# Kernel tuning notes

Measured on AMD Instinct MI355X. Metric: run time of the kernel, lower is better.

Reference implementation:

```python
import jax, jax.numpy as jnp
import numpy as np

B, N = 16, 64
EMB, CDIM, NL = 32, 24, 3      # emb_dim, cloud_dim, number of degrees l=0..2 (cloudord)
NBASIS, H, RADIUS = 10, 150, 2.0
BETA = 5.0                     # rescaled_act.Softplus(beta=5)


def sp(x):
    return jax.nn.softplus(BETA * x) / BETA


def cosine_basis(r):
    # CosineBasisModel: cos^2 bumps on centers linspace(0, max_radius, nbasis)
    centers = jnp.linspace(0.0, RADIUS, NBASIS).astype(r.dtype)
    step = RADIUS / (NBASIS - 1)
    d = (r[..., None] - centers) / step
    return jnp.where(jnp.abs(d) < 1.0, jnp.cos(0.5 * jnp.pi * d) ** 2, 0.0)


def sph_harm(u):
    # real spherical harmonics l=0,1,2 on unit vectors u[...,3]
    x, y, z = u[..., 0], u[..., 1], u[..., 2]
    Y0 = jnp.full(u.shape[:-1] + (1,), 0.28209479177387814, u.dtype)
    c1 = 0.4886025119029199
    Y1 = c1 * jnp.stack([y, z, x], -1)
    c2a, c2b, c2c = 1.0925484305920792, 0.31539156525252005, 0.5462742152960396
    Y2 = jnp.stack([c2a * x * y, c2a * y * z, c2b * (3 * z * z - 1.0),
                    c2a * x * z, c2c * (x * x - y * y)], -1)
    return [Y0, Y1, Y2]


def setup_inputs() -> dict:
    key = jax.random.key(0)
    ks = jax.random.split(key, 16)
    d = {}
    d['xyz'] = jax.random.normal(ks[0], (B, N, 3), jnp.float32)
    d['Z'] = jax.random.randint(ks[1], (B, N), 0, 6)
    d['body23'] = jax.random.normal(ks[2], (B, N, 3), jnp.float32)
    # embedding table (6 species)
    d['emb_W'] = jax.random.normal(ks[3], (6, EMB), jnp.float32) * 0.1
    # radial model MLP: NBASIS -> 150 -> 150 -> 150 -> NL*CDIM*EMB
    ROUT = NL * CDIM * EMB
    d['rW0'] = jax.random.normal(ks[4], (NBASIS, H), jnp.float32) / np.sqrt(NBASIS)
    d['rb0'] = jnp.zeros((H,), jnp.float32)
    d['rW1'] = jax.random.normal(ks[5], (H, H), jnp.float32) / np.sqrt(H)
    d['rb1'] = jnp.zeros((H,), jnp.float32)
    d['rW2'] = jax.random.normal(ks[6], (H, H), jnp.float32) / np.sqrt(H)
    d['rb2'] = jnp.zeros((H,), jnp.float32)
    d['rW3'] = jax.random.normal(ks[7], (H, ROUT), jnp.float32) / np.sqrt(H)
    d['rb3'] = jnp.zeros((ROUT,), jnp.float32)
    # AtomResiduals (1 block) on 219 channels
    CR = CDIM * NL * NL + 3  # 219
    d['res_W'] = jax.random.normal(ks[8], (CR, CR), jnp.float32) / np.sqrt(CR)
    d['res_b'] = jnp.zeros((CR,), jnp.float32)
    # collate: Linear(438,128) + BatchNorm1d(128)
    d['c_W'] = jax.random.normal(ks[9], (2 * CR, 128), jnp.float32) / np.sqrt(2 * CR)
    d['c_b'] = jnp.zeros((128,), jnp.float32)
    d['bn_g'] = jnp.ones((128,), jnp.float32)
    d['bn_b'] = jnp.zeros((128,), jnp.float32)
    # output layer
    d['o_W'] = jax.random.normal(ks[10], (128, 1), jnp.float32) / np.sqrt(128.0)
    d['o_b'] = jnp.zeros((1,), jnp.float32)
    return d


def reference(xyz, Z, body23, emb_W, rW0, rb0, rW1, rb1, rW2, rb2, rW3, rb3,
              res_W, res_b, c_W, c_b, bn_g, bn_b, o_W, o_b):
    f = emb_W[Z]                                        # [B,N,EMB] atom embeddings
    diff = xyz[:, :, None, :] - xyz[:, None, :, :]      # [B,N,N,3]
    r = jnp.sqrt(jnp.sum(diff * diff, -1) + 1e-12)      # [B,N,N]
    mask = ((r < RADIUS) & (r > 1e-6)).astype(f.dtype)  # neighbors within radius, no self
    u = diff / r[..., None]
    Ys = sph_harm(u)                                    # [ [B,N,N,1], [..,3], [..,5] ]
    # radial model on all pairs
    h = sp(cosine_basis(r) @ rW0 + rb0)
    h = sp(h @ rW1 + rb1)
    h = sp(h @ rW2 + rb2)
    R = (h @ rW3 + rb3).reshape(B, N, N, NL, CDIM, EMB)
    R = R * mask[..., None, None, None]
    # equivariant neighbor convolution: out[a,co,l,m] = sum_n,ci R_l(r_an) Y_lm(u_an) f[n,ci]
    outs = []
    for l in range(NL):
        o = jnp.einsum('banoi,banm,bni->baom', R[..., l, :, :], Ys[l], f)
        outs.append(o.reshape(B, N, -1) / jnp.sqrt(float(N)))
    feats = jnp.concatenate(outs, -1)                   # [B,N,216]
    feats = jnp.concatenate([body23, feats], -1)        # [B,N,219] (final_res concat)
    # AtomResiduals: concat(x, x + sp(Linear(x))) -> channel doubling
    res = feats + sp(feats @ res_W + res_b)
    feats = jnp.concatenate([feats, res], -1)           # [B,N,438]
    # lp_pool2d(norm_type=2, kernel=(N,1)): sqrt of sum of squares over atoms
    pooled = jnp.sqrt(jnp.sum(feats * feats, axis=1))   # [B,438]
    # collate: softplus(Linear), softplus(BatchNorm1d) (training-mode batch stats)
    hh = jax.nn.softplus(pooled @ c_W + c_b)
    mu = hh.mean(0)
    var = hh.var(0)
    hh = jax.nn.softplus((hh - mu) / jnp.sqrt(var + 1e-5) * bn_g + bn_b)
    return jax.nn.sigmoid(hh @ o_W + o_b)               # [B,1]
```

## Files before the change

### kernel.cpp

```cpp
#include <hip/hip_runtime.h>
#include <math.h>

constexpr int cB  = 16;
constexpr int cN  = 64;
constexpr int EMB = 32;
constexpr int NL  = 3;
constexpr int CDIM = 24;
constexpr int LOD = NL * CDIM;
constexpr int NB  = 10;
constexpr int H   = 150;
constexpr int CR  = 219;
constexpr int C2  = 438;
constexpr int HD  = 128;
constexpr int NSP = 6;
constexpr int GC  = NSP * LOD;
constexpr int GCP = 512;
constexpr int TBL = 512;
constexpr float RADIUS = 2.0f;

__device__ __forceinline__ float sp5(float x) {
    return fmaxf(x, 0.0f) + 0.2f * log1pf(expf(-5.0f * fabsf(x)));
}
__device__ __forceinline__ float sp1(float x) {
    return fmaxf(x, 0.0f) + log1pf(expf(-fabsf(x)));
}

__global__ void __launch_bounds__(256) k_prep(const float* __restrict__ emb_W,
                                              const float* __restrict__ rW3,
                                              const float* __restrict__ rb3,
                                              const float* __restrict__ c_W,
                                              const float* __restrict__ res_W,
                                              float* __restrict__ W2,
                                              float* __restrict__ Pbz,
                                              float* __restrict__ c_Wt,
                                              float* __restrict__ pooled2,
                                              float* __restrict__ partial,
                                              float* __restrict__ touch) {
    int bx = blockIdx.x;
    int t = threadIdx.x;
    __shared__ float e[EMB];
    if (bx < 90) {
        int z = bx / 15, hb = bx - (bx / 15) * 15;
        if (t < EMB) e[t] = emb_W[z * EMB + t];
        __syncthreads();
        for (int o = t; o < 10 * LOD; o += 256) {
            int k = hb * 10 + o / LOD, lo = o % LOD;
            const float* wr = &rW3[(size_t)k * (LOD * EMB) + lo * EMB];
            float s = 0.0f;
            #pragma unroll
            for (int i = 0; i < EMB; ++i) s = fmaf(wr[i], e[i], s);
            W2[(size_t)k * GCP + z * LOD + lo] = s;
        }
        if (z == 0) {
            for (int o = t; o < 10 * (GCP - GC); o += 256) {
                int k = hb * 10 + o / (GCP - GC), c = GC + o % (GCP - GC);
                W2[(size_t)k * GCP + c] = 0.0f;
            }
        }
        if (hb == 0 && t < LOD) {
            float s = 0.0f;
            #pragma unroll
            for (int i = 0; i < EMB; ++i) s = fmaf(rb3[t * EMB + i], e[i], s);
            Pbz[z * LOD + t] = s;
        }
    } else if (bx < 154) {
        int wb = bx - 90;
        const int n4 = (CR * CR) / 4;
        float s = 0.0f;
        for (int i = wb * 256 + t; i < n4; i += 64 * 256) {
            float4 v = *(const float4*)&res_W[4 * i];
            s += v.x + v.y + v.z + v.w;
        }
        touch[wb * 256 + t] = s;
    } else {
        int pb = bx - 154;
        int totalT = HD * 440;
        int total2 = totalT + cB * C2 + HD * 16 + 1;
        for (int i = pb * 256 + t; i < total2; i += 32 * 256) {
            if (i < totalT) {
                int jj = i / 440, ch = i - jj * 440;
                c_Wt[i] = (ch < C2) ? c_W[ch * HD + jj] : 0.0f;
            } else if (i < totalT + cB * C2) {
                pooled2[i - totalT] = 0.0f;
            } else {
                partial[i - totalT - cB * C2] = 0.0f;
            }
        }
    }
}

__global__ void __launch_bounds__(256) k_chain(const float* __restrict__ rW0,
                                               const float* __restrict__ rb0,
                                               const float* __restrict__ rW1,
                                               const float* __restrict__ rb1,
                                               const float* __restrict__ rW2,
                                               const float* __restrict__ rb2,
                                               const float* __restrict__ W2,
                                               const float* __restrict__ Pbz,
                                               float* __restrict__ G) {
    const int row0 = blockIdx.x * 2;
    const int t = threadIdx.x;
    const int a2 = t >> 7;
    const int jt = t & 127;
    const bool hasx = (jt < 22);
    const int jx = hasx ? 128 + jt : 128;

    __shared__ __align__(16) float bas[2][10];
    __shared__ __align__(16) float hA[2 * 152];
    __shared__ __align__(16) float hB[2 * 152];

    if (t < 2) {
        float r = (float)(row0 + t) * (RADIUS / (float)(TBL - 1));
        #pragma unroll
        for (int k = 0; k < NB; ++k) {
            float d = r * 4.5f - (float)k;
            float v = 0.0f;
            if (fabsf(d) < 1.0f) { float cc = cosf(1.57079632679489662f * d); v = cc * cc; }
            bas[t][k] = v;
        }
    }
    __syncthreads();

    {
        float a0 = 0, ax = 0;
        #pragma unroll
        for (int k = 0; k < NB; ++k) {
            float x = bas[a2][k];
            a0 = fmaf(x, rW0[k * H + jt], a0);
            ax = fmaf(x, rW0[k * H + jx], ax);
        }
        hA[a2 * 152 + jt] = sp5(a0 + rb0[jt]);
        if (hasx) hA[a2 * 152 + 128 + jt] = sp5(ax + rb0[128 + jt]);
    }
    __syncthreads();

    for (int layer = 0; layer < 2; ++layer) {
        const float* W   = layer ? rW2 : rW1;
        const float* bb  = layer ? rb2 : rb1;
        const float* src = layer ? hB : hA;
        float*       dst = layer ? hA : hB;
        float a0 = 0, ax = 0;
        const float* xs = &src[a2 * 152];
        #pragma unroll 10
        for (int k = 0; k < H; ++k) {
            float x = xs[k];
            const float* wr = &W[k * H];
            a0 = fmaf(x, wr[jt], a0);
            ax = fmaf(x, wr[jx], ax);
        }
        dst[a2 * 152 + jt] = sp5(a0 + bb[jt]);
        if (hasx) dst[a2 * 152 + 128 + jt] = sp5(ax + bb[128 + jt]);
        __syncthreads();
    }

    if (jt < 108) {
        const int g0 = 4 * jt;
        float4 c0 = {0, 0, 0, 0};
        const float* xs = &hA[a2 * 152];
        #pragma unroll 10
        for (int k = 0; k < H; ++k) {
            float x = xs[k];
            float4 w = *(const float4*)&W2[(size_t)k * GCP + g0];
            c0.x = fmaf(x, w.x, c0.x); c0.y = fmaf(x, w.y, c0.y);
            c0.z = fmaf(x, w.z, c0.z); c0.w = fmaf(x, w.w, c0.w);
        }
        int row = row0 + a2;
        float4 p = *(const float4*)&Pbz[g0];
        float4 o;
        o.x = c0.x + p.x; o.y = c0.y + p.y; o.z = c0.z + p.z; o.w = c0.w + p.w;
        *(float4*)&G[(size_t)row * GC + g0] = o;
    }
}

__global__ void __launch_bounds__(256) k_red(const float* __restrict__ xyz,
                                             const int* __restrict__ Z,
                                             const float* __restrict__ body23,
                                             const float* __restrict__ G,
                                             const float* __restrict__ res_W,
                                             const float* __restrict__ res_b,
                                             float* __restrict__ pooled2) {
    int ba = blockIdx.x;
    int b = ba >> 6, a = ba & 63;
    int t = threadIdx.x;
    __shared__ float ym[64][12];
    __shared__ float ymc[64][12];
    __shared__ __align__(16) float ps[64][76];
    __shared__ float xr[224];
    __shared__ int t0s[64];
    __shared__ float wls[64];
    __shared__ int zs[64];
    __shared__ int alist[64];
    __shared__ int cnt_s;
    if (t < 64) {
        int n = t;
        float ax = xyz[((size_t)b * cN + a) * 3 + 0];
        float ay = xyz[((size_t)b * cN + a) * 3 + 1];
        float az = xyz[((size_t)b * cN + a) * 3 + 2];
        float d0 = ax - xyz[((size_t)b * cN + n) * 3 + 0];
        float d1 = ay - xyz[((size_t)b * cN + n) * 3 + 1];
        float d2 = az - xyz[((size_t)b * cN + n) * 3 + 2];
        float s = d0 * d0 + d1 * d1 + d2 * d2;
        float r = sqrtf(s + 1e-12f);
        bool m = (r < RADIUS) && (r > 1e-6f);
        float u = r * ((float)(TBL - 1) / RADIUS);
        int t0 = (int)u;
        if (t0 > TBL - 2) t0 = TBL - 2;
        t0s[n] = t0;
        wls[n] = u - (float)t0;
        zs[n] = Z[b * cN + n];
        float inv = 1.0f / r;
        float x = d0 * inv, y = d1 * inv, z = d2 * inv;
        ym[n][0] = 0.28209479177387814f;
        ym[n][1] = 0.4886025119029199f * y;
        ym[n][2] = 0.4886025119029199f * z;
        ym[n][3] = 0.4886025119029199f * x;
        ym[n][4] = 1.0925484305920792f * x * y;
        ym[n][5] = 1.0925484305920792f * y * z;
        ym[n][6] = 0.31539156525252005f * (3.0f * z * z - 1.0f);
        ym[n][7] = 1.0925484305920792f * x * z;
        ym[n][8] = 0.5462742152960396f * (x * x - y * y);
        unsigned long long mask = __ballot(m);
        int rank = __popcll(mask & ((1ull << n) - 1ull));
        if (m) alist[rank] = n;
        if (n == 0) cnt_s = (int)__popcll(mask);
    }
    __syncthreads();
    int cnt = cnt_s;
    for (int i = t; i < cnt * 9; i += 256) {
        int ci = i / 9, yi = i - ci * 9;
        ymc[ci][yi] = ym[alist[ci]][yi];
    }
    for (int i = t; i < cnt * 18; i += 256) {
        int ci = i / 18, q = i - ci * 18;
        int n = alist[ci];
        const float* g = &G[(size_t)t0s[n] * GC + zs[n] * LOD + 4 * q];
        float4 g0 = *(const float4*)g;
        float4 g1 = *(const float4*)(g + GC);
        float wl = wls[n];
        float4 v;
        v.x = g0.x + wl * (g1.x - g0.x);
        v.y = g0.y + wl * (g1.y - g0.y);
        v.z = g0.z + wl * (g1.z - g0.z);
        v.w = g0.w + wl * (g1.w - g0.w);
        *(float4*)&ps[ci][4 * q] = v;
    }
    __syncthreads();
    if (t < 216) {
        int lo, yi;
        if (t < 24) { lo = t; yi = 0; }
        else if (t < 96) { int q = t - 24; int o = q / 3; lo = 24 + o; yi = 1 + (q - o * 3); }
        else { int q = t - 96; int o = q / 5; lo = 48 + o; yi = 4 + (q - o * 5); }
        float acc = 0.0f;
        #pragma unroll 4
        for (int ci = 0; ci < cnt; ++ci)
            acc = fmaf(ps[ci][lo], ymc[ci][yi], acc);
        xr[3 + t] = acc * 0.125f;
    } else if (t < 219) {
        xr[t - 216] = body23[(size_t)ba * 3 + (t - 216)];
    }
    __syncthreads();
    if (t < CR) {
        float xv = xr[t];
        float s = 0.0f;
        #pragma unroll 8
        for (int k = 0; k < CR; ++k)
            s = fmaf(xr[k], res_W[(size_t)k * CR + t], s);
        float o = xv + sp5(res_b[t] + s);
        atomicAdd(&pooled2[b * C2 + t],      xv * xv);
        atomicAdd(&pooled2[b * C2 + CR + t], o * o);
    }
}

__global__ void __launch_bounds__(64) k_headm(const float* __restrict__ pooled2,
                                              const float* __restrict__ c_Wt,
                                              const float* __restrict__ c_b,
                                              const float* __restrict__ bn_g,
                                              const float* __restrict__ bn_b,
                                              const float* __restrict__ o_W,
                                              const float* __restrict__ o_b,
                                              float* __restrict__ partial,
                                              float* __restrict__ out) {
    int j = blockIdx.x;
    int l = threadIdx.x;
    float acc[cB];
    #pragma unroll
    for (int b = 0; b < cB; ++b) acc[b] = 0.0f;
    const float* wr = &c_Wt[j * 440];
    for (int ch = l; ch < C2; ch += 64) {
        float wv = wr[ch];
        #pragma unroll
        for (int b = 0; b < cB; ++b)
            acc[b] = fmaf(sqrtf(pooled2[b * C2 + ch]), wv, acc[b]);
    }
    #pragma unroll
    for (int off = 32; off >= 1; off >>= 1) {
        #pragma unroll
        for (int b = 0; b < cB; ++b) acc[b] += __shfl_xor(acc[b], off, 64);
    }
    __shared__ int is_last;
    if (l == 0) {
        float cb = c_b[j];
        float h[cB];
        float mu = 0.0f;
        #pragma unroll
        for (int b = 0; b < cB; ++b) { h[b] = sp1(acc[b] + cb); mu += h[b]; }
        mu *= (1.0f / cB);
        float var = 0.0f;
        #pragma unroll
        for (int b = 0; b < cB; ++b) { float d = h[b] - mu; var = fmaf(d, d, var); }
        var *= (1.0f / cB);
        float sc = bn_g[j] / sqrtf(var + 1e-5f);
        float bnb = bn_b[j];
        float ow = o_W[j];
        #pragma unroll
        for (int b = 0; b < cB; ++b)
            partial[j * cB + b] = sp1((h[b] - mu) * sc + bnb) * ow;
        __threadfence();
        unsigned int old = atomicAdd((unsigned int*)&partial[HD * cB], 1u);
        is_last = (old == (unsigned int)(HD - 1));
    }
    __syncthreads();
    if (is_last) {
        int bcol = l & 15, grp = l >> 4;
        float s = 0.0f;
        #pragma unroll 8
        for (int jr = grp * 32; jr < grp * 32 + 32; ++jr)
            s += partial[jr * cB + bcol];
        s += __shfl_down(s, 32, 64);
        s += __shfl_down(s, 16, 64);
        if (l < cB)
            out[l] = 1.0f / (1.0f + expf(-(s + o_b[0])));
    }
}

extern "C" void kernel_launch(void* const* d_in, const int* in_sizes, int n_in,
                              void* d_out, int out_size, void* d_ws, size_t ws_size,
                              hipStream_t stream) {
    const float* xyz    = (const float*)d_in[0];
    const int*   Z      = (const int*)d_in[1];
    const float* body23 = (const float*)d_in[2];
    const float* emb_W  = (const float*)d_in[3];
    const float* rW0    = (const float*)d_in[4];
    const float* rb0    = (const float*)d_in[5];
    const float* rW1    = (const float*)d_in[6];
    const float* rb1    = (const float*)d_in[7];
    const float* rW2    = (const float*)d_in[8];
    const float* rb2    = (const float*)d_in[9];
    const float* rW3    = (const float*)d_in[10];
    const float* rb3    = (const float*)d_in[11];
    const float* res_W  = (const float*)d_in[12];
    const float* res_b  = (const float*)d_in[13];
    const float* c_W    = (const float*)d_in[14];
    const float* c_b    = (const float*)d_in[15];
    const float* bn_g   = (const float*)d_in[16];
    const float* bn_b   = (const float*)d_in[17];
    const float* o_W    = (const float*)d_in[18];
    const float* o_b    = (const float*)d_in[19];

    float* w       = (float*)d_ws;
    float* W2      = w;
    float* Pbz     = W2 + 76800;
    float* c_Wt    = Pbz + 432;
    float* G       = c_Wt + 56320;
    float* pooled2 = G + 221184;
    float* partial = pooled2 + 7008;
    float* touch   = partial + 2080;
    (void)in_sizes; (void)n_in; (void)out_size; (void)ws_size;

    k_prep <<<186, 256, 0, stream>>>(emb_W, rW3, rb3, c_W, res_W,
                                     W2, Pbz, c_Wt, pooled2, partial, touch);
    k_chain<<<TBL / 2, 256, 0, stream>>>(rW0, rb0, rW1, rb1, rW2, rb2, W2, Pbz, G);
    k_red  <<<cB * cN, 256, 0, stream>>>(xyz, Z, body23, G, res_W, res_b, pooled2);
    k_headm<<<HD, 64, 0, stream>>>(pooled2, c_Wt, c_b, bn_g, bn_b, o_W, o_b,
                                   partial, (float*)d_out);
}
```

Baseline: 61.40 us.

## Process one radial table row per block in k_chain instead of two

Remaps k_chain so that each block computes the MLP chain for a single radial-table row, with threads 0..149 each owning one hidden unit. The grid doubles from 256 to 512 blocks. Before, each block handled two rows and split them across 128-thread halves, with extra columns covered by a second accumulator. The aim is more parallelism across the GPU and less per-thread serial work. In exchange, 106 of 256 threads sit idle, weight loads are no longer shared between two rows, and an extra barrier is added per layer.

```diff
diff --git a/kernel.cpp b/kernel.cpp
--- a/kernel.cpp
+++ b/kernel.cpp
@@ -98,39 +98,31 @@
                                                const float* __restrict__ W2,
                                                const float* __restrict__ Pbz,
                                                float* __restrict__ G) {
-    const int row0 = blockIdx.x * 2;
+    const int row = blockIdx.x;
     const int t = threadIdx.x;
-    const int a2 = t >> 7;
-    const int jt = t & 127;
-    const bool hasx = (jt < 22);
-    const int jx = hasx ? 128 + jt : 128;
-
-    __shared__ __align__(16) float bas[2][10];
-    __shared__ __align__(16) float hA[2 * 152];
-    __shared__ __align__(16) float hB[2 * 152];
-
-    if (t < 2) {
-        float r = (float)(row0 + t) * (RADIUS / (float)(TBL - 1));
+
+    __shared__ __align__(16) float bas[10];
+    __shared__ __align__(16) float hA[152];
+    __shared__ __align__(16) float hB[152];
+
+    if (t == 0) {
+        float r = (float)row * (RADIUS / (float)(TBL - 1));
         #pragma unroll
         for (int k = 0; k < NB; ++k) {
             float d = r * 4.5f - (float)k;
             float v = 0.0f;
             if (fabsf(d) < 1.0f) { float cc = cosf(1.57079632679489662f * d); v = cc * cc; }
-            bas[t][k] = v;
-        }
-    }
-    __syncthreads();
-
-    {
-        float a0 = 0, ax = 0;
-        #pragma unroll
-        for (int k = 0; k < NB; ++k) {
-            float x = bas[a2][k];
-            a0 = fmaf(x, rW0[k * H + jt], a0);
-            ax = fmaf(x, rW0[k * H + jx], ax);
-        }
-        hA[a2 * 152 + jt] = sp5(a0 + rb0[jt]);
-        if (hasx) hA[a2 * 152 + 128 + jt] = sp5(ax + rb0[128 + jt]);
+            bas[k] = v;
+        }
+    }
+    __syncthreads();
+
+    if (t < H) {
+        float a0 = 0;
+        #pragma unroll
+        for (int k = 0; k < NB; ++k)
+            a0 = fmaf(bas[k], rW0[k * H + t], a0);
+        hA[t] = sp5(a0 + rb0[t]);
     }
     __syncthreads();
 
@@ -139,32 +131,27 @@
         const float* bb  = layer ? rb2 : rb1;
         const float* src = layer ? hB : hA;
         float*       dst = layer ? hA : hB;
-        float a0 = 0, ax = 0;
-        const float* xs = &src[a2 * 152];
+        float a0 = 0;
+        if (t < H) {
+            #pragma unroll 10
+            for (int k = 0; k < H; ++k)
+                a0 = fmaf(src[k], W[k * H + t], a0);
+        }
+        __syncthreads();
+        if (t < H) dst[t] = sp5(a0 + bb[t]);
+        __syncthreads();
+    }
+
+    if (t < 108) {
+        const int g0 = 4 * t;
+        float4 c0 = {0, 0, 0, 0};
         #pragma unroll 10
         for (int k = 0; k < H; ++k) {
-            float x = xs[k];
-            const float* wr = &W[k * H];
-            a0 = fmaf(x, wr[jt], a0);
-            ax = fmaf(x, wr[jx], ax);
-        }
-        dst[a2 * 152 + jt] = sp5(a0 + bb[jt]);
-        if (hasx) dst[a2 * 152 + 128 + jt] = sp5(ax + bb[128 + jt]);
-        __syncthreads();
-    }
-
-    if (jt < 108) {
-        const int g0 = 4 * jt;
-        float4 c0 = {0, 0, 0, 0};
-        const float* xs = &hA[a2 * 152];
-        #pragma unroll 10
-        for (int k = 0; k < H; ++k) {
-            float x = xs[k];
+            float x = hA[k];
             float4 w = *(const float4*)&W2[(size_t)k * GCP + g0];
             c0.x = fmaf(x, w.x, c0.x); c0.y = fmaf(x, w.y, c0.y);
             c0.z = fmaf(x, w.z, c0.z); c0.w = fmaf(x, w.w, c0.w);
         }
-        int row = row0 + a2;
         float4 p = *(const float4*)&Pbz[g0];
         float4 o;
         o.x = c0.x + p.x; o.y = c0.y + p.y; o.z = c0.z + p.z; o.w = c0.w + p.w;
@@ -369,7 +356,7 @@
 
     k_prep <<<186, 256, 0, stream>>>(emb_W, rW3, rb3, c_W, res_W,
                                      W2, Pbz, c_Wt, pooled2, partial, touch);
-    k_chain<<<TBL / 2, 256, 0, stream>>>(rW0, rb0, rW1, rb1, rW2, rb2, W2, Pbz, G);
+    k_chain<<<TBL, 256, 0, stream>>>(rW0, rb0, rW1, rb1, rW2, rb2, W2, Pbz, G);
     k_red  <<<cB * cN, 256, 0, stream>>>(xyz, Z, body23, G, res_W, res_b, pooled2);
     k_headm<<<HD, 64, 0, stream>>>(pooled2, c_Wt, c_b, bn_g, bn_b, o_W, o_b,
                                    partial, (float*)d_out);
```

New measurement: 59.46 us. 3.2% less time.
